# Kernel tuning notes

Measured on AMD Instinct MI355X. Metric: run time of the kernel, lower is better.

Reference implementation:

```python
import jax, jax.numpy as jnp
import numpy as np

N_NODES = 100000
N_EDGES = 1600000
D_IN = 128
D_OUT = 128


def setup_inputs() -> dict:
    key = jax.random.key(0)
    k1, k2, k3, k4 = jax.random.split(key, 4)
    x = jax.random.normal(k1, (N_NODES, D_IN), dtype=jnp.float32)
    edge_index = jax.random.randint(k2, (2, N_EDGES), 0, N_NODES, dtype=jnp.int64)
    # PyTorch Linear default init: U(-1/sqrt(fan_in), 1/sqrt(fan_in))
    bound = 1.0 / np.sqrt(D_IN)
    W1 = jax.random.uniform(k3, (D_OUT, D_IN), minval=-bound, maxval=bound, dtype=jnp.float32)
    W2 = jax.random.uniform(k4, (D_OUT, D_IN), minval=-bound, maxval=bound, dtype=jnp.float32)
    return {"x": x, "edge_index": edge_index, "W1": W1, "W2": W2}


def reference(x, edge_index, W1, W2):
    # self transform: [N, D_out]
    self_features = x @ W1.T
    # neighbor transform: [N, D_out]
    neighbor_features = x @ W2.T
    row, col = edge_index[0], edge_index[1]
    # gather by source (col), scatter-add by destination (row)
    aggregated = jax.ops.segment_sum(neighbor_features[col], row, num_segments=x.shape[0])
    return jax.nn.relu(self_features + aggregated)
```

## Files before the change

### kernel.cpp

```cpp
#include <hip/hip_runtime.h>

#define N_NODES 100000
#define DIM 128
#define NBIN 391
#define BINSZ 256
#define NCH 782
#define CHUNK 2048
#define FCAP 24
#define SLOTS (NBIN * FCAP)
#define ENTCAP 4608
#define FSPB 128
#define SSPB 256

typedef __attribute__((ext_vector_type(8))) short bf16x8;
typedef __attribute__((ext_vector_type(4))) float f32x4;

__device__ __forceinline__ unsigned short f2bf(float f) {
  unsigned u = __builtin_bit_cast(unsigned, f);
  u += 0x7fff + ((u >> 16) & 1);
  return (unsigned short)(u >> 16);
}
__device__ __forceinline__ float bfhi(unsigned u) {
  return __builtin_bit_cast(float, u & 0xffff0000u);
}
__device__ __forceinline__ float bflo(unsigned u) {
  return __builtin_bit_cast(float, u << 16);
}

__global__ __launch_bounds__(256, 4) void fill_kernel(
    const int* __restrict__ rows, const int* __restrict__ cols,
    int* __restrict__ counts, unsigned* __restrict__ binned,
    int* __restrict__ fspillc, int2* __restrict__ fspill, int n_edges,
    const float* __restrict__ W1, const float* __restrict__ W2,
    unsigned short* __restrict__ Wb) {
  const int tid = threadIdx.x;
  if (blockIdx.x >= NCH) {
    const int v = (blockIdx.x - NCH) * 256 + tid;
    const int j = v >> 5, q = v & 31;
    const float* Wrow =
        (j < 128) ? (W1 + (size_t)j * DIM) : (W2 + (size_t)(j - 128) * DIM);
    const float4 val = *(const float4*)(Wrow + 4 * q);
    const unsigned lo = (unsigned)f2bf(val.x) | ((unsigned)f2bf(val.y) << 16);
    const unsigned hi = (unsigned)f2bf(val.z) | ((unsigned)f2bf(val.w) << 16);
    *(uint2*)(Wb + (size_t)j * DIM + 4 * q) = make_uint2(lo, hi);
    return;
  }

  __shared__ unsigned buf[SLOTS];
  __shared__ int lcnt[NBIN];
  __shared__ int fsc;
  const int ch = blockIdx.x;
  for (int i = tid; i < NBIN; i += 256) lcnt[i] = 0;
  if (tid == 0) fsc = 0;
  __syncthreads();

  const int e0 = ch * CHUNK + tid * 8;
  int rv[8], cv[8];
  int nval;
  if (e0 + 8 <= n_edges) {
    *(int4*)&rv[0] = *(const int4*)(rows + e0);
    *(int4*)&rv[4] = *(const int4*)(rows + e0 + 4);
    *(int4*)&cv[0] = *(const int4*)(cols + e0);
    *(int4*)&cv[4] = *(const int4*)(cols + e0 + 4);
    nval = 8;
  } else {
    nval = 0;
    for (int k = 0; k < 8; ++k)
      if (e0 + k < n_edges) {
        rv[nval] = rows[e0 + k];
        cv[nval] = cols[e0 + k];
        ++nval;
      }
  }
  for (int k = 0; k < nval; ++k) {
    const int r = rv[k];
    const int b = r >> 8;
    const unsigned payload = ((unsigned)(r & 255) << 17) | (unsigned)cv[k];
    const int slot = atomicAdd(&lcnt[b], 1);
    if (slot < FCAP) {
      buf[b * FCAP + slot] = payload;
    } else {
      const int sp = atomicAdd(&fsc, 1);
      if (sp < FSPB) fspill[ch * FSPB + sp] = make_int2(r, cv[k]);
    }
  }
  __syncthreads();

  unsigned* dst = binned + (size_t)ch * SLOTS;
  for (int i4 = tid; i4 < SLOTS / 4; i4 += 256)
    *(uint4*)(dst + 4 * i4) = *(const uint4*)&buf[4 * i4];
  for (int b = tid; b < NBIN; b += 256)
    counts[(size_t)ch * NBIN + b] = min(lcnt[b], FCAP);
  if (tid == 0) fspillc[ch] = min(fsc, FSPB);
}

__global__ __launch_bounds__(256, 2) void gemm_kernel(
    const float* __restrict__ x, const unsigned short* __restrict__ Wb,
    unsigned short* __restrict__ selfb, unsigned short* __restrict__ neigh) {
  __shared__ unsigned short xs[128 * 136];

  const int tid = threadIdx.x;
  const int lane = tid & 63;
  const int w = tid >> 6;
  const int nb = blockIdx.x * 128;
  const int quad = lane >> 4;
  const int l15 = lane & 15;

  bf16x8 bfrag[4][4];
#pragma unroll
  for (int nt = 0; nt < 4; ++nt) {
    const int j = w * 64 + nt * 16 + l15;
#pragma unroll
    for (int ks = 0; ks < 4; ++ks)
      bfrag[nt][ks] =
          *(const bf16x8*)(Wb + (size_t)j * DIM + ks * 32 + quad * 8);
  }

#pragma unroll
  for (int half = 0; half < 2; ++half) {
    float4 av[8];
#pragma unroll
    for (int it = 0; it < 8; ++it) {
      const int v = tid + (half * 8 + it) * 256;
      const int m = v >> 5, q = v & 31;
      av[it] = (nb + m < N_NODES)
                   ? *(const float4*)(x + (size_t)(nb + m) * DIM + 4 * q)
                   : make_float4(0.f, 0.f, 0.f, 0.f);
    }
#pragma unroll
    for (int it = 0; it < 8; ++it) {
      const int v = tid + (half * 8 + it) * 256;
      const int m = v >> 5, q = v & 31;
      const unsigned lo =
          (unsigned)f2bf(av[it].x) | ((unsigned)f2bf(av[it].y) << 16);
      const unsigned hi =
          (unsigned)f2bf(av[it].z) | ((unsigned)f2bf(av[it].w) << 16);
      *(uint2*)&xs[m * 136 + 4 * q] = make_uint2(lo, hi);
    }
  }
  __syncthreads();

  f32x4 acc[8][4];
#pragma unroll
  for (int mt = 0; mt < 8; ++mt)
#pragma unroll
    for (int nt = 0; nt < 4; ++nt) acc[mt][nt] = (f32x4){0.f, 0.f, 0.f, 0.f};

#pragma unroll
  for (int ks = 0; ks < 4; ++ks) {
#pragma unroll
    for (int mt = 0; mt < 8; ++mt) {
      const bf16x8 afrag =
          *(const bf16x8*)&xs[(mt * 16 + l15) * 136 + ks * 32 + quad * 8];
#pragma unroll
      for (int nt = 0; nt < 4; ++nt)
        acc[mt][nt] = __builtin_amdgcn_mfma_f32_16x16x32_bf16(
            afrag, bfrag[nt][ks], acc[mt][nt], 0, 0, 0);
    }
  }

#pragma unroll
  for (int h = 0; h < 2; ++h) {
    __syncthreads();
    if ((w >> 1) == h) {
#pragma unroll
      for (int mt = 0; mt < 8; ++mt)
#pragma unroll
        for (int nt = 0; nt < 4; ++nt) {
          const int col = (w & 1) * 64 + nt * 16 + l15;
#pragma unroll
          for (int r = 0; r < 4; ++r)
            xs[(mt * 16 + quad * 4 + r) * 136 + col] = f2bf(acc[mt][nt][r]);
        }
    }
    __syncthreads();
    unsigned short* dst = h ? neigh : selfb;
#pragma unroll
    for (int it = 0; it < 8; ++it) {
      const int v = it * 256 + tid;
      const int row = v >> 4, q = v & 15;
      if (nb + row < N_NODES)
        *(uint4*)(dst + (size_t)(nb + row) * DIM + 8 * q) =
            *(const uint4*)&xs[row * 136 + 8 * q];
    }
  }
}

__global__ __launch_bounds__(256, 3) void sort_kernel(
    const int* __restrict__ counts, const unsigned* __restrict__ binned,
    int* __restrict__ csr_cols, int* __restrict__ row_ptr,
    int* __restrict__ degs, int* __restrict__ sspillc,
    int2* __restrict__ sspill) {
  __shared__ int segc[NCH];
  __shared__ int ssa[NCH], ssb[NCH];
  __shared__ unsigned entbuf[ENTCAP];
  __shared__ int outbuf[ENTCAP];
  __shared__ int hist[BINSZ], hsa[BINSZ], hsb[BINSZ], cur[BINSZ];
  __shared__ int ssc;

  const int tid = threadIdx.x;
  const int bin = blockIdx.x;
  if (tid == 0) ssc = 0;

  for (int i = tid; i < NCH; i += 256) {
    const int c = counts[(size_t)i * NBIN + bin];
    segc[i] = c;
    ssa[i] = c;
  }
  __syncthreads();
  for (int off = 1; off < NCH; off <<= 1) {
    for (int i = tid; i < NCH; i += 256)
      ssb[i] = ssa[i] + ((i >= off) ? ssa[i - off] : 0);
    __syncthreads();
    for (int i = tid; i < NCH; i += 256) ssa[i] = ssb[i];
    __syncthreads();
  }

  const unsigned* bbase = binned + (size_t)bin * FCAP;
  for (int u = tid; u < NCH * (FCAP / 4); u += 256) {
    const int ch = u / 6;
    const int q = u - ch * 6;
    uint4 v4 = *(const uint4*)(bbase + (size_t)ch * SLOTS + 4 * q);
    const int cnt = segc[ch];
    const int base = ssa[ch] - cnt;
    const unsigned vals[4] = {v4.x, v4.y, v4.z, v4.w};
#pragma unroll
    for (int j = 0; j < 4; ++j) {
      const int slot = 4 * q + j;
      if (slot < cnt) {
        const int pos = base + slot;
        if (pos < ENTCAP) {
          entbuf[pos] = vals[j];
        } else {
          const int sp = atomicAdd(&ssc, 1);
          if (sp < SSPB)
            sspill[bin * SSPB + sp] = make_int2(
                (bin << 8) | (int)(vals[j] >> 17), (int)(vals[j] & 0x1FFFFu));
        }
      }
    }
  }
  hist[tid] = 0;
  __syncthreads();

  const int total = min(ssa[NCH - 1], ENTCAP);
  for (int i = tid; i < total; i += 256) atomicAdd(&hist[entbuf[i] >> 17], 1);
  __syncthreads();

  hsa[tid] = hist[tid];
  __syncthreads();
  for (int off = 1; off < BINSZ; off <<= 1) {
    hsb[tid] = hsa[tid] + ((tid >= off) ? hsa[tid - off] : 0);
    __syncthreads();
    hsa[tid] = hsb[tid];
    __syncthreads();
  }

  const int gbase = bin * ENTCAP;
  {
    const int start = hsa[tid] - hist[tid];
    cur[tid] = start;
    const int node = (bin << 8) | tid;
    if (node < N_NODES) {
      row_ptr[node] = gbase + start;
      degs[node] = hist[tid];
    }
  }
  __syncthreads();

  for (int i = tid; i < total; i += 256) {
    const unsigned p = entbuf[i];
    const int pos = atomicAdd(&cur[p >> 17], 1);
    outbuf[pos] = (int)(p & 0x1FFFFu);
  }
  __syncthreads();

  for (int i = tid; i < total; i += 256) csr_cols[gbase + i] = outbuf[i];
  if (tid == 0) sspillc[bin] = min(ssc, SSPB);
}

__global__ __launch_bounds__(256) void agg_kernel(
    const int* __restrict__ row_ptr, const int* __restrict__ degs,
    const int* __restrict__ csr_cols, const unsigned short* __restrict__ neigh,
    const unsigned short* __restrict__ selfb, const int* __restrict__ fspillc,
    const int2* __restrict__ fspill, const int* __restrict__ sspillc,
    const int2* __restrict__ sspill, float* __restrict__ out) {
  __shared__ int has_spill;
  const int tid = threadIdx.x;
  if (tid == 0) has_spill = 0;
  __syncthreads();
  for (int i = tid; i < NCH + NBIN; i += 256) {
    const int v = (i < NCH) ? fspillc[i] : sspillc[i - NCH];
    if (v) atomicOr(&has_spill, 1);
  }
  __syncthreads();
  const bool spilled = has_spill != 0;

  const int l = tid & 63;
  const int wid = blockIdx.x * 4 + (tid >> 6);
  const int stride = gridDim.x * 4;
  const unsigned* ng = (const unsigned*)neigh;

  for (int node = wid; node < N_NODES; node += stride) {
    const int deg = degs[node];
    const int* cl = csr_cols + row_ptr[node];
    const unsigned s = ((const unsigned*)selfb)[(size_t)node * 64 + l];

    float ax = 0.f, ay = 0.f;
    int d = 0;
    for (; d + 8 <= deg; d += 8) {
      unsigned uv[8];
#pragma unroll
      for (int k = 0; k < 8; ++k) uv[k] = ng[(size_t)cl[d + k] * 64 + l];
#pragma unroll
      for (int k = 0; k < 8; ++k) {
        ax += bflo(uv[k]);
        ay += bfhi(uv[k]);
      }
    }
    const int rem = deg - d;
    if (rem) {
      unsigned uv[8];
      const int cdup = cl[d];
#pragma unroll
      for (int k = 0; k < 8; ++k) {
        const int ci = (k < rem) ? cl[d + k] : cdup;
        uv[k] = ng[(size_t)ci * 64 + l];
      }
#pragma unroll
      for (int k = 0; k < 8; ++k) {
        if (k < rem) {
          ax += bflo(uv[k]);
          ay += bfhi(uv[k]);
        }
      }
    }

    if (spilled) {
      for (int bi = 0; bi < NCH; ++bi) {
        const int n = min(fspillc[bi], FSPB);
        for (int i = 0; i < n; ++i) {
          const int2 e = fspill[bi * FSPB + i];
          if (e.x == node) {
            const unsigned u = ng[(size_t)e.y * 64 + l];
            ax += bflo(u);
            ay += bfhi(u);
          }
        }
      }
      for (int bi = 0; bi < NBIN; ++bi) {
        const int n = min(sspillc[bi], SSPB);
        for (int i = 0; i < n; ++i) {
          const int2 e = sspill[bi * SSPB + i];
          if (e.x == node) {
            const unsigned u = ng[(size_t)e.y * 64 + l];
            ax += bflo(u);
            ay += bfhi(u);
          }
        }
      }
    }

    float2 o;
    o.x = fmaxf(bflo(s) + ax, 0.f);
    o.y = fmaxf(bfhi(s) + ay, 0.f);
    *(float2*)(out + (size_t)node * DIM + 2 * l) = o;
  }
}

extern "C" void kernel_launch(void* const* d_in, const int* in_sizes, int n_in,
                              void* d_out, int out_size, void* d_ws,
                              size_t ws_size, hipStream_t stream) {
  const float* x = (const float*)d_in[0];
  const int* edge_index = (const int*)d_in[1];
  const float* W1 = (const float*)d_in[2];
  const float* W2 = (const float*)d_in[3];
  float* out = (float*)d_out;

  const int n_edges = in_sizes[1] / 2;
  const int* rows = edge_index;
  const int* cols = edge_index + n_edges;

  char* p = (char*)d_ws;
  unsigned short* selfb = (unsigned short*)p;
  p += (size_t)N_NODES * DIM * 2;
  unsigned short* neigh = (unsigned short*)p;
  p += (size_t)N_NODES * DIM * 2;
  unsigned* binned = (unsigned*)p;
  p += (size_t)NCH * SLOTS * 4;
  int* counts = (int*)p;
  p += (size_t)NCH * NBIN * 4;
  int* csr_cols = (int*)p;
  p += (size_t)NBIN * ENTCAP * 4;
  int* row_ptr = (int*)p;
  p += (size_t)N_NODES * 4;
  int* degs = (int*)p;
  p += (size_t)N_NODES * 4;
  int* fspillc = (int*)p;
  p += 4096;
  int2* fspill = (int2*)p;
  p += (size_t)NCH * FSPB * sizeof(int2);
  int* sspillc = (int*)p;
  p += 4096;
  int2* sspill = (int2*)p;
  p += (size_t)NBIN * SSPB * sizeof(int2);
  unsigned short* Wb = (unsigned short*)p;

  fill_kernel<<<NCH + 32, 256, 0, stream>>>(rows, cols, counts, binned,
                                            fspillc, fspill, n_edges, W1, W2,
                                            Wb);
  gemm_kernel<<<(N_NODES + 127) / 128, 256, 0, stream>>>(x, Wb, selfb, neigh);
  sort_kernel<<<NBIN, 256, 0, stream>>>(counts, binned, csr_cols, row_ptr,
                                        degs, sspillc, sspill);
  agg_kernel<<<2048, 256, 0, stream>>>(row_ptr, degs, csr_cols, neigh, selfb,
                                       fspillc, fspill, sspillc, sspill, out);
}
```

Baseline: 233.5 us.

## Fuse GEMM and per-bin sort into one kernel with interleaved block roles

Merges the dense bf16 GEMM kernel and the per-bin CSR sort kernel into a single launch, assigning two of every three blocks to GEMM tiles and one to a sort bin. Shared memory is unioned between the two roles. This removes one kernel launch and its drain and tail, and lets the MFMA-heavy GEMM overlap with the latency- and LDS-bound sort. The tradeoff is that occupancy is now set by the larger shared footprint and the GEMM launch bounds, which may reduce how many sort blocks run at once.

```diff
diff --git a/kernel.cpp b/kernel.cpp
--- a/kernel.cpp
+++ b/kernel.cpp
@@ -11,6 +11,7 @@
 #define ENTCAP 4608
 #define FSPB 128
 #define SSPB 256
+#define NGEMM 782
 
 typedef __attribute__((ext_vector_type(8))) short bf16x8;
 typedef __attribute__((ext_vector_type(4))) float f32x4;
@@ -94,189 +95,198 @@
   if (tid == 0) fspillc[ch] = min(fsc, FSPB);
 }
 
-__global__ __launch_bounds__(256, 2) void gemm_kernel(
+union FusedSh {
+  unsigned short xs[128 * 136];
+  struct {
+    int segc[NCH], ssa[NCH], ssb[NCH];
+    unsigned entbuf[ENTCAP];
+    int outbuf[ENTCAP];
+    int hist[BINSZ], hsa[BINSZ], hsb[BINSZ], cur[BINSZ];
+    int ssc;
+  } s;
+};
+
+__global__ __launch_bounds__(256, 2) void gemmsort_kernel(
     const float* __restrict__ x, const unsigned short* __restrict__ Wb,
-    unsigned short* __restrict__ selfb, unsigned short* __restrict__ neigh) {
-  __shared__ unsigned short xs[128 * 136];
-
-  const int tid = threadIdx.x;
-  const int lane = tid & 63;
-  const int w = tid >> 6;
-  const int nb = blockIdx.x * 128;
-  const int quad = lane >> 4;
-  const int l15 = lane & 15;
-
-  bf16x8 bfrag[4][4];
-#pragma unroll
-  for (int nt = 0; nt < 4; ++nt) {
-    const int j = w * 64 + nt * 16 + l15;
-#pragma unroll
-    for (int ks = 0; ks < 4; ++ks)
-      bfrag[nt][ks] =
-          *(const bf16x8*)(Wb + (size_t)j * DIM + ks * 32 + quad * 8);
-  }
-
-#pragma unroll
-  for (int half = 0; half < 2; ++half) {
-    float4 av[8];
-#pragma unroll
-    for (int it = 0; it < 8; ++it) {
-      const int v = tid + (half * 8 + it) * 256;
-      const int m = v >> 5, q = v & 31;
-      av[it] = (nb + m < N_NODES)
-                   ? *(const float4*)(x + (size_t)(nb + m) * DIM + 4 * q)
-                   : make_float4(0.f, 0.f, 0.f, 0.f);
-    }
-#pragma unroll
-    for (int it = 0; it < 8; ++it) {
-      const int v = tid + (half * 8 + it) * 256;
-      const int m = v >> 5, q = v & 31;
-      const unsigned lo =
-          (unsigned)f2bf(av[it].x) | ((unsigned)f2bf(av[it].y) << 16);
-      const unsigned hi =
-          (unsigned)f2bf(av[it].z) | ((unsigned)f2bf(av[it].w) << 16);
-      *(uint2*)&xs[m * 136 + 4 * q] = make_uint2(lo, hi);
-    }
-  }
-  __syncthreads();
-
-  f32x4 acc[8][4];
-#pragma unroll
-  for (int mt = 0; mt < 8; ++mt)
-#pragma unroll
-    for (int nt = 0; nt < 4; ++nt) acc[mt][nt] = (f32x4){0.f, 0.f, 0.f, 0.f};
-
-#pragma unroll
-  for (int ks = 0; ks < 4; ++ks) {
-#pragma unroll
-    for (int mt = 0; mt < 8; ++mt) {
-      const bf16x8 afrag =
-          *(const bf16x8*)&xs[(mt * 16 + l15) * 136 + ks * 32 + quad * 8];
-#pragma unroll
-      for (int nt = 0; nt < 4; ++nt)
-        acc[mt][nt] = __builtin_amdgcn_mfma_f32_16x16x32_bf16(
-            afrag, bfrag[nt][ks], acc[mt][nt], 0, 0, 0);
-    }
-  }
-
-#pragma unroll
-  for (int h = 0; h < 2; ++h) {
-    __syncthreads();
-    if ((w >> 1) == h) {
-#pragma unroll
-      for (int mt = 0; mt < 8; ++mt)
-#pragma unroll
-        for (int nt = 0; nt < 4; ++nt) {
-          const int col = (w & 1) * 64 + nt * 16 + l15;
-#pragma unroll
-          for (int r = 0; r < 4; ++r)
-            xs[(mt * 16 + quad * 4 + r) * 136 + col] = f2bf(acc[mt][nt][r]);
-        }
-    }
-    __syncthreads();
-    unsigned short* dst = h ? neigh : selfb;
-#pragma unroll
-    for (int it = 0; it < 8; ++it) {
-      const int v = it * 256 + tid;
-      const int row = v >> 4, q = v & 15;
-      if (nb + row < N_NODES)
-        *(uint4*)(dst + (size_t)(nb + row) * DIM + 8 * q) =
-            *(const uint4*)&xs[row * 136 + 8 * q];
-    }
-  }
-}
-
-__global__ __launch_bounds__(256, 3) void sort_kernel(
+    unsigned short* __restrict__ selfb, unsigned short* __restrict__ neigh,
     const int* __restrict__ counts, const unsigned* __restrict__ binned,
     int* __restrict__ csr_cols, int* __restrict__ row_ptr,
     int* __restrict__ degs, int* __restrict__ sspillc,
     int2* __restrict__ sspill) {
-  __shared__ int segc[NCH];
-  __shared__ int ssa[NCH], ssb[NCH];
-  __shared__ unsigned entbuf[ENTCAP];
-  __shared__ int outbuf[ENTCAP];
-  __shared__ int hist[BINSZ], hsa[BINSZ], hsb[BINSZ], cur[BINSZ];
-  __shared__ int ssc;
-
+  __shared__ FusedSh sh;
   const int tid = threadIdx.x;
-  const int bin = blockIdx.x;
-  if (tid == 0) ssc = 0;
-
-  for (int i = tid; i < NCH; i += 256) {
-    const int c = counts[(size_t)i * NBIN + bin];
-    segc[i] = c;
-    ssa[i] = c;
-  }
-  __syncthreads();
-  for (int off = 1; off < NCH; off <<= 1) {
-    for (int i = tid; i < NCH; i += 256)
-      ssb[i] = ssa[i] + ((i >= off) ? ssa[i - off] : 0);
-    __syncthreads();
-    for (int i = tid; i < NCH; i += 256) ssa[i] = ssb[i];
-    __syncthreads();
-  }
-
-  const unsigned* bbase = binned + (size_t)bin * FCAP;
-  for (int u = tid; u < NCH * (FCAP / 4); u += 256) {
-    const int ch = u / 6;
-    const int q = u - ch * 6;
-    uint4 v4 = *(const uint4*)(bbase + (size_t)ch * SLOTS + 4 * q);
-    const int cnt = segc[ch];
-    const int base = ssa[ch] - cnt;
-    const unsigned vals[4] = {v4.x, v4.y, v4.z, v4.w};
-#pragma unroll
-    for (int j = 0; j < 4; ++j) {
-      const int slot = 4 * q + j;
-      if (slot < cnt) {
-        const int pos = base + slot;
-        if (pos < ENTCAP) {
-          entbuf[pos] = vals[j];
-        } else {
-          const int sp = atomicAdd(&ssc, 1);
-          if (sp < SSPB)
-            sspill[bin * SSPB + sp] = make_int2(
-                (bin << 8) | (int)(vals[j] >> 17), (int)(vals[j] & 0x1FFFFu));
+  const int g = blockIdx.x / 3, r3 = blockIdx.x % 3;
+
+  if (r3 < 2) {
+    const int t = g * 2 + r3;
+    const int lane = tid & 63;
+    const int w = tid >> 6;
+    const int nb = t * 128;
+    const int quad = lane >> 4;
+    const int l15 = lane & 15;
+
+    bf16x8 bfrag[4][4];
+#pragma unroll
+    for (int nt = 0; nt < 4; ++nt) {
+      const int j = w * 64 + nt * 16 + l15;
+#pragma unroll
+      for (int ks = 0; ks < 4; ++ks)
+        bfrag[nt][ks] =
+            *(const bf16x8*)(Wb + (size_t)j * DIM + ks * 32 + quad * 8);
+    }
+
+#pragma unroll
+    for (int half = 0; half < 2; ++half) {
+      float4 av[8];
+#pragma unroll
+      for (int it = 0; it < 8; ++it) {
+        const int v = tid + (half * 8 + it) * 256;
+        const int m = v >> 5, q = v & 31;
+        av[it] = (nb + m < N_NODES)
+                     ? *(const float4*)(x + (size_t)(nb + m) * DIM + 4 * q)
+                     : make_float4(0.f, 0.f, 0.f, 0.f);
+      }
+#pragma unroll
+      for (int it = 0; it < 8; ++it) {
+        const int v = tid + (half * 8 + it) * 256;
+        const int m = v >> 5, q = v & 31;
+        const unsigned lo =
+            (unsigned)f2bf(av[it].x) | ((unsigned)f2bf(av[it].y) << 16);
+        const unsigned hi =
+            (unsigned)f2bf(av[it].z) | ((unsigned)f2bf(av[it].w) << 16);
+        *(uint2*)&sh.xs[m * 136 + 4 * q] = make_uint2(lo, hi);
+      }
+    }
+    __syncthreads();
+
+    f32x4 acc[8][4];
+#pragma unroll
+    for (int mt = 0; mt < 8; ++mt)
+#pragma unroll
+      for (int nt = 0; nt < 4; ++nt) acc[mt][nt] = (f32x4){0.f, 0.f, 0.f, 0.f};
+
+#pragma unroll
+    for (int ks = 0; ks < 4; ++ks) {
+#pragma unroll
+      for (int mt = 0; mt < 8; ++mt) {
+        const bf16x8 afrag =
+            *(const bf16x8*)&sh.xs[(mt * 16 + l15) * 136 + ks * 32 + quad * 8];
+#pragma unroll
+        for (int nt = 0; nt < 4; ++nt)
+          acc[mt][nt] = __builtin_amdgcn_mfma_f32_16x16x32_bf16(
+              afrag, bfrag[nt][ks], acc[mt][nt], 0, 0, 0);
+      }
+    }
+
+#pragma unroll
+    for (int h = 0; h < 2; ++h) {
+      __syncthreads();
+      if ((w >> 1) == h) {
+#pragma unroll
+        for (int mt = 0; mt < 8; ++mt)
+#pragma unroll
+          for (int nt = 0; nt < 4; ++nt) {
+            const int col = (w & 1) * 64 + nt * 16 + l15;
+#pragma unroll
+            for (int r = 0; r < 4; ++r)
+              sh.xs[(mt * 16 + quad * 4 + r) * 136 + col] =
+                  f2bf(acc[mt][nt][r]);
+          }
+      }
+      __syncthreads();
+      unsigned short* dst = h ? neigh : selfb;
+#pragma unroll
+      for (int it = 0; it < 8; ++it) {
+        const int v = it * 256 + tid;
+        const int row = v >> 4, q = v & 15;
+        if (nb + row < N_NODES)
+          *(uint4*)(dst + (size_t)(nb + row) * DIM + 8 * q) =
+              *(const uint4*)&sh.xs[row * 136 + 8 * q];
+      }
+    }
+  } else {
+    const int bin = g;
+    if (tid == 0) sh.s.ssc = 0;
+
+    for (int i = tid; i < NCH; i += 256) {
+      const int c = counts[(size_t)i * NBIN + bin];
+      sh.s.segc[i] = c;
+      sh.s.ssa[i] = c;
+    }
+    __syncthreads();
+    for (int off = 1; off < NCH; off <<= 1) {
+      for (int i = tid; i < NCH; i += 256)
+        sh.s.ssb[i] = sh.s.ssa[i] + ((i >= off) ? sh.s.ssa[i - off] : 0);
+      __syncthreads();
+      for (int i = tid; i < NCH; i += 256) sh.s.ssa[i] = sh.s.ssb[i];
+      __syncthreads();
+    }
+
+    const unsigned* bbase = binned + (size_t)bin * FCAP;
+    for (int u = tid; u < NCH * (FCAP / 4); u += 256) {
+      const int ch = u / 6;
+      const int q = u - ch * 6;
+      uint4 v4 = *(const uint4*)(bbase + (size_t)ch * SLOTS + 4 * q);
+      const int cnt = sh.s.segc[ch];
+      const int base = sh.s.ssa[ch] - cnt;
+      const unsigned vals[4] = {v4.x, v4.y, v4.z, v4.w};
+#pragma unroll
+      for (int j = 0; j < 4; ++j) {
+        const int slot = 4 * q + j;
+        if (slot < cnt) {
+          const int pos = base + slot;
+          if (pos < ENTCAP) {
+            sh.s.entbuf[pos] = vals[j];
+          } else {
+            const int sp = atomicAdd(&sh.s.ssc, 1);
+            if (sp < SSPB)
+              sspill[bin * SSPB + sp] =
+                  make_int2((bin << 8) | (int)(vals[j] >> 17),
+                            (int)(vals[j] & 0x1FFFFu));
+          }
         }
       }
     }
-  }
-  hist[tid] = 0;
-  __syncthreads();
-
-  const int total = min(ssa[NCH - 1], ENTCAP);
-  for (int i = tid; i < total; i += 256) atomicAdd(&hist[entbuf[i] >> 17], 1);
-  __syncthreads();
-
-  hsa[tid] = hist[tid];
-  __syncthreads();
-  for (int off = 1; off < BINSZ; off <<= 1) {
-    hsb[tid] = hsa[tid] + ((tid >= off) ? hsa[tid - off] : 0);
-    __syncthreads();
-    hsa[tid] = hsb[tid];
-    __syncthreads();
-  }
-
-  const int gbase = bin * ENTCAP;
-  {
-    const int start = hsa[tid] - hist[tid];
-    cur[tid] = start;
-    const int node = (bin << 8) | tid;
-    if (node < N_NODES) {
-      row_ptr[node] = gbase + start;
-      degs[node] = hist[tid];
-    }
-  }
-  __syncthreads();
-
-  for (int i = tid; i < total; i += 256) {
-    const unsigned p = entbuf[i];
-    const int pos = atomicAdd(&cur[p >> 17], 1);
-    outbuf[pos] = (int)(p & 0x1FFFFu);
-  }
-  __syncthreads();
-
-  for (int i = tid; i < total; i += 256) csr_cols[gbase + i] = outbuf[i];
-  if (tid == 0) sspillc[bin] = min(ssc, SSPB);
+    sh.s.hist[tid] = 0;
+    __syncthreads();
+
+    const int total = min(sh.s.ssa[NCH - 1], ENTCAP);
+    for (int i = tid; i < total; i += 256)
+      atomicAdd(&sh.s.hist[sh.s.entbuf[i] >> 17], 1);
+    __syncthreads();
+
+    sh.s.hsa[tid] = sh.s.hist[tid];
+    __syncthreads();
+    for (int off = 1; off < BINSZ; off <<= 1) {
+      sh.s.hsb[tid] = sh.s.hsa[tid] + ((tid >= off) ? sh.s.hsa[tid - off] : 0);
+      __syncthreads();
+      sh.s.hsa[tid] = sh.s.hsb[tid];
+      __syncthreads();
+    }
+
+    const int gbase = bin * ENTCAP;
+    {
+      const int start = sh.s.hsa[tid] - sh.s.hist[tid];
+      sh.s.cur[tid] = start;
+      const int node = (bin << 8) | tid;
+      if (node < N_NODES) {
+        row_ptr[node] = gbase + start;
+        degs[node] = sh.s.hist[tid];
+      }
+    }
+    __syncthreads();
+
+    for (int i = tid; i < total; i += 256) {
+      const unsigned p = sh.s.entbuf[i];
+      const int pos = atomicAdd(&sh.s.cur[p >> 17], 1);
+      sh.s.outbuf[pos] = (int)(p & 0x1FFFFu);
+    }
+    __syncthreads();
+
+    for (int i = tid; i < total; i += 256)
+      csr_cols[gbase + i] = sh.s.outbuf[i];
+    if (tid == 0) sspillc[bin] = min(sh.s.ssc, SSPB);
+  }
 }
 
 __global__ __launch_bounds__(256) void agg_kernel(
@@ -409,9 +419,9 @@
   fill_kernel<<<NCH + 32, 256, 0, stream>>>(rows, cols, counts, binned,
                                             fspillc, fspill, n_edges, W1, W2,
                                             Wb);
-  gemm_kernel<<<(N_NODES + 127) / 128, 256, 0, stream>>>(x, Wb, selfb, neigh);
-  sort_kernel<<<NBIN, 256, 0, stream>>>(counts, binned, csr_cols, row_ptr,
-                                        degs, sspillc, sspill);
+  gemmsort_kernel<<<3 * NBIN, 256, 0, stream>>>(x, Wb, selfb, neigh, counts,
+                                                binned, csr_cols, row_ptr,
+                                                degs, sspillc, sspill);
   agg_kernel<<<2048, 256, 0, stream>>>(row_ptr, degs, csr_cols, neigh, selfb,
                                        fspillc, fspill, sspillc, sspill, out);
 }
```

Result: no change. 232.2 us (-0.6%).
